# Optimization experiments

Hardware: AMD Instinct MI355X
Metric: run time of the kernel (lower is better)

The kernel has to match this reference:

```python
import jax, jax.numpy as jnp
import numpy as np

B, S, HID, QK, H = 2, 2048, 2048, 2048, 16
DK, DV = QK // H, HID // H
EPS = 1e-5


def setup_inputs() -> dict:
    key = jax.random.key(0)
    ks = jax.random.split(key, 8)
    sd = 1.0 / np.sqrt(HID)
    inp = {
        "x": jax.random.normal(ks[0], (B, S, HID), jnp.float32),
        "wq": jax.random.normal(ks[1], (HID, QK), jnp.float32) * sd,
        "bq": jnp.zeros((QK,), jnp.float32),
        "wk": jax.random.normal(ks[2], (HID, QK), jnp.float32) * sd,
        "bk": jnp.zeros((QK,), jnp.float32),
        "wv": jax.random.normal(ks[3], (HID, HID), jnp.float32) * sd,
        "bv": jnp.zeros((HID,), jnp.float32),
        "wg": jax.random.normal(ks[4], (HID, HID), jnp.float32) * sd,
        "bg": jnp.zeros((HID,), jnp.float32),
        "wo": jax.random.normal(ks[5], (HID, HID), jnp.float32) * sd,
        "bo": jnp.zeros((HID,), jnp.float32),
        "gn_w": jnp.ones((HID,), jnp.float32),
        "gn_b": jnp.zeros((HID,), jnp.float32),
        # RetNet default gammas: 1 - exp(linspace(log(1/32), log(1/512), H))
        "gamma": 1.0 - jnp.exp(jnp.linspace(-np.log(32.0), -np.log(512.0), H)).astype(jnp.float32),
    }
    return inp


def reference(x, wq, bq, wk, bk, wv, bv, wg, bg, wo, bo, gn_w, gn_b, gamma):
    b, s, hid = x.shape
    h = gamma.shape[0]
    dk = wq.shape[1] // h
    dv = hid // h
    # projections + head split -> (b, h, s, d)
    q = (x @ wq + bq).reshape(b, s, h, dk).transpose(0, 2, 1, 3)
    k = (x @ wk + bk).reshape(b, s, h, dk).transpose(0, 2, 1, 3)
    v = (x @ wv + bv).reshape(b, s, h, dv).transpose(0, 2, 1, 3)
    # causal decay mask: gamma^(n-m) for n >= m else 0  -> (h, s, s)
    idx = jnp.arange(s)
    diff = idx[:, None] - idx[None, :]
    expn = jnp.maximum(diff, 0).astype(x.dtype)
    dmask = jnp.where(diff >= 0, gamma[:, None, None] ** expn, 0.0)
    # parallel retention
    scores = jnp.einsum('bhnd,bhmd->bhnm', q, k) * dmask
    ret = jnp.einsum('bhnm,bhmv->bhnv', scores, v)  # (b, h, s, dv)
    # GroupNorm(num_groups=h) over (b, hid, s): stats per (b, head) over (s, dv)
    mean = ret.mean(axis=(2, 3), keepdims=True)
    var = ((ret - mean) ** 2).mean(axis=(2, 3), keepdims=True)
    norm = (ret - mean) * jax.lax.rsqrt(var + EPS)
    norm = norm * gn_w.reshape(h, dv)[None, :, None, :] + gn_b.reshape(h, dv)[None, :, None, :]
    ro = norm.transpose(0, 2, 1, 3).reshape(b, s, hid)  # (b, s, hid)
    gate = jax.nn.silu(x @ wg + bg)
    out = (gate * ro) @ wo + bo
    return out
```

## Files before the change

### kernel.cpp

```cpp
#include <hip/hip_runtime.h>
#include <cstdint>
#include <cstddef>

#define DEVI __device__ __forceinline__

typedef unsigned short u16;
typedef __bf16 bf16_t;
typedef bf16_t bf16x8 __attribute__((ext_vector_type(8)));
typedef float f32x4 __attribute__((ext_vector_type(4)));

constexpr int BB = 2, SS = 2048, HID = 2048, NH = 16, DK = 128, DV = 128;
constexpr int KD = HID;

DEVI u16 f2bf(float f) {
  union { float f; uint32_t u; } v; v.f = f;
  uint32_t u = v.u;
  uint32_t r = u + 0x7FFFu + ((u >> 16) & 1u);
  return (u16)(r >> 16);
}
DEVI float bf2f(u16 h) {
  union { uint32_t u; float f; } v; v.u = ((uint32_t)h) << 16;
  return v.f;
}
DEVI f32x4 mfma16(bf16x8 a, bf16x8 b, f32x4 c) {
  return __builtin_amdgcn_mfma_f32_16x16x32_bf16(a, b, c, 0, 0, 0);
}
DEVI void gload16(const u16* g, u16* l) {
  __builtin_amdgcn_global_load_lds(
      (const __attribute__((address_space(1))) uint32_t*)g,
      (__attribute__((address_space(3))) uint32_t*)l, 16, 0, 0);
}

__global__ __launch_bounds__(256) void castx_kernel(
    const float* __restrict__ x, u16* __restrict__ xb)
{
  size_t i = ((size_t)blockIdx.x * 256 + threadIdx.x) * 8;
  float4 a = *(const float4*)(x + i);
  float4 b = *(const float4*)(x + i + 4);
  ushort4 lo, hi;
  lo.x = f2bf(a.x); lo.y = f2bf(a.y); lo.z = f2bf(a.z); lo.w = f2bf(a.w);
  hi.x = f2bf(b.x); hi.y = f2bf(b.y); hi.z = f2bf(b.z); hi.w = f2bf(b.w);
  *(ushort4*)(xb + i) = lo;
  *(ushort4*)(xb + i + 4) = hi;
}

__global__ __launch_bounds__(256) void wtrans_kernel(
    const float* __restrict__ wq, const float* __restrict__ wk,
    const float* __restrict__ wv, const float* __restrict__ wg,
    const float* __restrict__ wo, u16* __restrict__ wt)
{
  __shared__ float t[32][33];
  const float* srcs[5] = {wq, wk, wv, wg, wo};
  const float* W = srcs[blockIdx.z];
  u16* dst = wt + (size_t)blockIdx.z * (size_t)KD * HID;
  int tx = threadIdx.x, ty = threadIdx.y;
  int c0 = blockIdx.x * 32, r0 = blockIdx.y * 32;
#pragma unroll
  for (int i = 0; i < 4; ++i)
    t[ty + i * 8][tx] = W[(size_t)(r0 + ty + i * 8) * HID + c0 + tx];
  __syncthreads();
#pragma unroll
  for (int i = 0; i < 4; ++i) {
    int n = c0 + ty + i * 8;
    int k = r0 + tx;
    dst[(size_t)n * KD + k] = f2bf(t[tx][ty + i * 8]);
  }
}

DEVI void stage256(const u16* __restrict__ A, const u16* __restrict__ Bt,
                   int m0, int n0, int kt, u16* sa, u16* sb, int tid)
{
#pragma unroll
  for (int i = 0; i < 4; ++i) {
    int c = i * 512 + tid;
    int row = c >> 3, scol = c & 7, dcol = scol ^ (row & 7);
    gload16(A + (size_t)(m0 + row) * KD + kt * 64 + dcol * 8, sa + c * 8);
  }
#pragma unroll
  for (int i = 0; i < 4; ++i) {
    int c = i * 512 + tid;
    int row = c >> 3, scol = c & 7, dcol = scol ^ (row & 7);
    gload16(Bt + (size_t)(n0 + row) * KD + kt * 64 + dcol * 8, sb + c * 8);
  }
}

DEVI void gemm256(const u16* __restrict__ A, const u16* __restrict__ Bt,
                  int m0, int n0, char* smem, f32x4 (&acc)[8][4])
{
  const int tid = threadIdx.x, lane = tid & 63, wave = tid >> 6;
  const int wr = wave >> 2, wc = wave & 3;
  const int lhi = lane >> 4, llo = lane & 15;

  stage256(A, Bt, m0, n0, 0, (u16*)smem, (u16*)(smem + 65536), tid);
  asm volatile("s_waitcnt vmcnt(0)" ::: "memory");
  __syncthreads();

  for (int kt = 0; kt < KD / 64; ++kt) {
    char* cA = smem + (kt & 1) * 32768;
    char* cB = smem + 65536 + (kt & 1) * 32768;
    if (kt + 1 < KD / 64) {
      u16* nA = (u16*)(smem + ((kt + 1) & 1) * 32768);
      u16* nB = (u16*)(smem + 65536 + ((kt + 1) & 1) * 32768);
      stage256(A, Bt, m0, n0, kt + 1, nA, nB, tid);
    }
    __builtin_amdgcn_s_setprio(1);
#pragma unroll
    for (int ks = 0; ks < 2; ++ks) {
      const int kb = ks * 64 + lhi * 16;
      bf16x8 bfr[4];
#pragma unroll
      for (int ni = 0; ni < 4; ++ni) {
        int row = wc * 64 + ni * 16 + llo;
        bfr[ni] = *(const bf16x8*)(cB + row * 128 + (kb ^ ((row & 7) << 4)));
      }
#pragma unroll
      for (int mi = 0; mi < 8; ++mi) {
        int row = wr * 128 + mi * 16 + llo;
        bf16x8 af = *(const bf16x8*)(cA + row * 128 + (kb ^ ((row & 7) << 4)));
#pragma unroll
        for (int ni = 0; ni < 4; ++ni)
          acc[mi][ni] = mfma16(af, bfr[ni], acc[mi][ni]);
      }
    }
    __builtin_amdgcn_s_setprio(0);
    asm volatile("s_waitcnt vmcnt(0)" ::: "memory");
    __syncthreads();
  }
}

__global__ __launch_bounds__(512, 2) void proj_kernel(
    const u16* __restrict__ xb, const u16* __restrict__ wtBase,
    const float* __restrict__ bq, const float* __restrict__ bk,
    const float* __restrict__ bv, const float* __restrict__ bg,
    u16* __restrict__ qb, u16* __restrict__ kb,
    u16* __restrict__ vtb, u16* __restrict__ gb)
{
  __shared__ __align__(16) char smem[131072];
  const int z = blockIdx.z;
  const u16* Bt = wtBase + (size_t)z * (size_t)KD * HID;
  f32x4 acc[8][4];
  const f32x4 zero = {0.f, 0.f, 0.f, 0.f};
#pragma unroll
  for (int mi = 0; mi < 8; ++mi)
#pragma unroll
    for (int ni = 0; ni < 4; ++ni) acc[mi][ni] = zero;

  const int m0 = blockIdx.x * 256, n0 = blockIdx.y * 256;
  gemm256(xb, Bt, m0, n0, smem, acc);

  const int tid = threadIdx.x, lane = tid & 63, wave = tid >> 6;
  const int wr = wave >> 2, wc = wave & 3;
  const int lhi = lane >> 4, llo = lane & 15;
  const float* bias = (z == 0) ? bq : (z == 1) ? bk : (z == 2) ? bv : bg;

  if (z == 2) {
#pragma unroll
    for (int mi = 0; mi < 8; ++mi) {
#pragma unroll
      for (int ni = 0; ni < 4; ++ni) {
        int row0 = m0 + wr * 128 + mi * 16 + lhi * 4;
        int n = n0 + wc * 64 + ni * 16 + llo;
        float bsn = bias[n];
        int b = row0 >> 11, s0 = row0 & (SS - 1);
        int h = n >> 7, j = n & 127;
        ushort4 hv;
        hv.x = f2bf(acc[mi][ni][0] + bsn);
        hv.y = f2bf(acc[mi][ni][1] + bsn);
        hv.z = f2bf(acc[mi][ni][2] + bsn);
        hv.w = f2bf(acc[mi][ni][3] + bsn);
        *(ushort4*)(vtb + ((size_t)((b * NH + h) * DV + j)) * SS + s0) = hv;
      }
    }
  } else {
    u16* Lb = (u16*)smem;
#pragma unroll
    for (int mi = 0; mi < 8; ++mi) {
#pragma unroll
      for (int ni = 0; ni < 4; ++ni) {
        int colL = wc * 64 + ni * 16 + llo;
        float bsn = bias[n0 + colL];
#pragma unroll
        for (int r = 0; r < 4; ++r) {
          int rowL = wr * 128 + mi * 16 + lhi * 4 + r;
          float c = acc[mi][ni][r] + bsn;
          if (z == 3) c = c / (1.0f + expf(-c));
          Lb[rowL * 256 + (colL ^ (((rowL >> 2) & 3) << 4))] = f2bf(c);
        }
      }
    }
    __syncthreads();
    int rr = tid & 255, chh = tid >> 8;
    int m = m0 + rr, b = m >> 11, s = m & (SS - 1);
    int swz = ((rr >> 2) & 3) << 4;
#pragma unroll
    for (int jj = 0; jj < 16; ++jj) {
      int c0 = chh * 128 + jj * 8;
      uint4 v = *(const uint4*)&Lb[rr * 256 + (c0 ^ swz)];
      int n = n0 + c0;
      if (z == 3) {
        *(uint4*)(gb + (size_t)m * HID + n) = v;
      } else {
        int h = n >> 7, j2 = n & 127;
        u16* dst = (z == 0) ? qb : kb;
        *(uint4*)(dst + ((size_t)((b * NH + h) * SS + s)) * DK + j2) = v;
      }
    }
  }
}

__global__ __launch_bounds__(256) void retention_kernel(
    const u16* __restrict__ qb, const u16* __restrict__ kb,
    const u16* __restrict__ vtb, const float* __restrict__ gamma,
    float* __restrict__ ret, float* __restrict__ stats)
{
  __shared__ __align__(16) char smemR[81920];
  __shared__ float red[8];

  const int bh = blockIdx.y;
  const int n0 = blockIdx.x * 128;
  const int h = bh & (NH - 1);
  const float lg2 = log2f(gamma[h]);

  const int tid = threadIdx.x, lane = tid & 63, wave = tid >> 6;
  const int lhi = lane >> 4, llo = lane & 15;
  const int qrow = n0 + wave * 32;

  const u16* qbase = qb + ((size_t)bh * SS + qrow) * DK;
  bf16x8 aq[2][4];
#pragma unroll
  for (int mi = 0; mi < 2; ++mi)
#pragma unroll
    for (int ks = 0; ks < 4; ++ks)
      aq[mi][ks] = *(const bf16x8*)(qbase + (size_t)(mi * 16 + llo) * DK + ks * 32 + lhi * 8);

  float rdec[2][4];
#pragma unroll
  for (int mi = 0; mi < 2; ++mi)
#pragma unroll
    for (int r = 0; r < 4; ++r)
      rdec[mi][r] = exp2f(lg2 * (float)(qrow + mi * 16 + lhi * 4 + r));

  const f32x4 zero = {0.f, 0.f, 0.f, 0.f};
  f32x4 oacc[2][8];
#pragma unroll
  for (int mi = 0; mi < 2; ++mi)
#pragma unroll
    for (int nj = 0; nj < 8; ++nj) oacc[mi][nj] = zero;

  const u16* kbase = kb + (size_t)bh * SS * DK;
  const u16* vbase = vtb + (size_t)bh * DV * SS;
  const int mtiles = n0 / 64 + 2;

  auto stageKV = [&](int mbase, u16* sk, u16* sv) {
#pragma unroll
    for (int i = 0; i < 4; ++i) {
      int c = i * 256 + tid;
      int row = c >> 4, scol = c & 15, dcol = scol ^ (row & 15);
      gload16(kbase + (size_t)(mbase + row) * DK + dcol * 8, sk + c * 8);
    }
#pragma unroll
    for (int i = 0; i < 4; ++i) {
      int c = i * 256 + tid;
      int row = c >> 3, scol = c & 7, dcol = scol ^ (row & 7);
      gload16(vbase + (size_t)row * SS + mbase + dcol * 8, sv + c * 8);
    }
  };

  stageKV(0, (u16*)smemR, (u16*)(smemR + 32768));
  asm volatile("s_waitcnt vmcnt(0)" ::: "memory");
  __syncthreads();

  for (int mt = 0; mt < mtiles; ++mt) {
    const int m0 = mt * 64;
    char* cK = smemR + (mt & 1) * 16384;
    char* cV = smemR + 32768 + (mt & 1) * 16384;
    if (mt + 1 < mtiles)
      stageKV(m0 + 64, (u16*)(smemR + ((mt + 1) & 1) * 16384),
              (u16*)(smemR + 32768 + ((mt + 1) & 1) * 16384));

    f32x4 sacc[2][4];
#pragma unroll
    for (int mi = 0; mi < 2; ++mi)
#pragma unroll
      for (int ni = 0; ni < 4; ++ni) sacc[mi][ni] = zero;
    __builtin_amdgcn_s_setprio(1);
#pragma unroll
    for (int ks = 0; ks < 4; ++ks) {
      const int kbyte = ks * 64 + lhi * 16;
      bf16x8 bk_[4];
#pragma unroll
      for (int ni = 0; ni < 4; ++ni) {
        int row = ni * 16 + llo;
        bk_[ni] = *(const bf16x8*)(cK + row * 256 + (kbyte ^ ((row & 15) << 4)));
      }
#pragma unroll
      for (int mi = 0; mi < 2; ++mi)
#pragma unroll
        for (int ni = 0; ni < 4; ++ni)
          sacc[mi][ni] = mfma16(aq[mi][ks], bk_[ni], sacc[mi][ni]);
    }
    __builtin_amdgcn_s_setprio(0);

    float cfac[4];
#pragma unroll
    for (int ni = 0; ni < 4; ++ni)
      cfac[ni] = exp2f(-lg2 * (float)(m0 + ni * 16 + llo));
    const bool masked = (m0 + 63 > qrow);
    char* myP = smemR + 65536 + wave * 4096;
#pragma unroll
    for (int mi = 0; mi < 2; ++mi) {
#pragma unroll
      for (int ni = 0; ni < 4; ++ni) {
#pragma unroll
        for (int r = 0; r < 4; ++r) {
          int prow = mi * 16 + lhi * 4 + r;
          int pcol = ni * 16 + llo;
          float w = rdec[mi][r] * cfac[ni];
          if (masked && (qrow + prow < m0 + pcol)) w = 0.0f;
          float p = sacc[mi][ni][r] * w;
          *(u16*)(myP + prow * 128 + ((pcol * 2) ^ ((prow & 7) << 4))) = f2bf(p);
        }
      }
    }

    __builtin_amdgcn_s_setprio(1);
#pragma unroll
    for (int ks2 = 0; ks2 < 2; ++ks2) {
      const int kbyte = ks2 * 64 + lhi * 16;
      bf16x8 pa[2];
#pragma unroll
      for (int mi = 0; mi < 2; ++mi) {
        int row = mi * 16 + llo;
        pa[mi] = *(const bf16x8*)(myP + row * 128 + (kbyte ^ ((row & 7) << 4)));
      }
#pragma unroll
      for (int nj = 0; nj < 8; ++nj) {
        int row = nj * 16 + llo;
        bf16x8 vb = *(const bf16x8*)(cV + row * 128 + (kbyte ^ ((row & 7) << 4)));
#pragma unroll
        for (int mi = 0; mi < 2; ++mi)
          oacc[mi][nj] = mfma16(pa[mi], vb, oacc[mi][nj]);
      }
    }
    __builtin_amdgcn_s_setprio(0);
    asm volatile("s_waitcnt vmcnt(0)" ::: "memory");
    __syncthreads();
  }

  float lsum = 0.f, lsq = 0.f;
  float* rbase = ret + ((size_t)bh * SS + qrow) * DV;
#pragma unroll
  for (int mi = 0; mi < 2; ++mi) {
#pragma unroll
    for (int nj = 0; nj < 8; ++nj) {
      int prow0 = mi * 16 + lhi * 4;
      int j = nj * 16 + llo;
#pragma unroll
      for (int r = 0; r < 4; ++r) {
        float v = oacc[mi][nj][r];
        rbase[(size_t)(prow0 + r) * DV + j] = v;
        lsum += v; lsq += v * v;
      }
    }
  }
#pragma unroll
  for (int off = 32; off > 0; off >>= 1) {
    lsum += __shfl_down(lsum, off, 64);
    lsq  += __shfl_down(lsq,  off, 64);
  }
  if (lane == 0) { red[wave * 2] = lsum; red[wave * 2 + 1] = lsq; }
  __syncthreads();
  if (tid == 0) {
    float s = red[0] + red[2] + red[4] + red[6];
    float q = red[1] + red[3] + red[5] + red[7];
    atomicAdd(&stats[bh * 2], s);
    atomicAdd(&stats[bh * 2 + 1], q);
  }
}

__global__ __launch_bounds__(256) void normgate_kernel(
    const float* __restrict__ ret, const u16* __restrict__ gb,
    const float* __restrict__ stats, const float* __restrict__ gn_w,
    const float* __restrict__ gn_b, u16* __restrict__ a2)
{
  const int idx4 = (blockIdx.x * 256 + threadIdx.x) * 4;
  const int bh = idx4 >> 18;
  const int rem = idx4 & (SS * DV - 1);
  const int s = rem >> 7;
  const int dv = rem & (DV - 1);
  const float inv = 1.0f / (float)(SS * DV);
  float mean = stats[bh * 2] * inv;
  float var = stats[bh * 2 + 1] * inv - mean * mean;
  float rstd = rsqrtf(var + 1e-5f);
  const int b = bh >> 4, h = bh & (NH - 1);
  const int hd = h * DV + dv;
  float4 rv = *(const float4*)(ret + idx4);
  float4 w4 = *(const float4*)(gn_w + hd);
  float4 b4 = *(const float4*)(gn_b + hd);
  size_t gidx = ((size_t)(b * SS + s)) * HID + hd;
  ushort4 g4 = *(const ushort4*)(gb + gidx);
  ushort4 o;
  o.x = f2bf(bf2f(g4.x) * ((rv.x - mean) * rstd * w4.x + b4.x));
  o.y = f2bf(bf2f(g4.y) * ((rv.y - mean) * rstd * w4.y + b4.y));
  o.z = f2bf(bf2f(g4.z) * ((rv.z - mean) * rstd * w4.z + b4.z));
  o.w = f2bf(bf2f(g4.w) * ((rv.w - mean) * rstd * w4.w + b4.w));
  *(ushort4*)(a2 + gidx) = o;
}

__global__ __launch_bounds__(512, 2) void final_kernel(
    const u16* __restrict__ a2, const u16* __restrict__ woT,
    const float* __restrict__ bo, float* __restrict__ out)
{
  __shared__ __align__(16) char smem[131072];
  f32x4 acc[8][4];
  const f32x4 zero = {0.f, 0.f, 0.f, 0.f};
#pragma unroll
  for (int mi = 0; mi < 8; ++mi)
#pragma unroll
    for (int ni = 0; ni < 4; ++ni) acc[mi][ni] = zero;

  const int m0 = blockIdx.x * 256, n0 = blockIdx.y * 256;
  gemm256(a2, woT, m0, n0, smem, acc);

  const int tid = threadIdx.x, lane = tid & 63, wave = tid >> 6;
  const int wr = wave >> 2, wc = wave & 3;
  const int lhi = lane >> 4, llo = lane & 15;
  float* Lf = (float*)smem;

#pragma unroll
  for (int pass = 0; pass < 2; ++pass) {
    if ((wc >> 1) == pass) {
#pragma unroll
      for (int mi = 0; mi < 8; ++mi) {
#pragma unroll
        for (int ni = 0; ni < 4; ++ni) {
          int colL = (wc & 1) * 64 + ni * 16 + llo;
          float bn = bo[n0 + pass * 128 + colL];
#pragma unroll
          for (int r = 0; r < 4; ++r) {
            int rowL = wr * 128 + mi * 16 + lhi * 4 + r;
            Lf[rowL * 128 + (colL ^ (((rowL >> 2) & 1) << 4))] =
                acc[mi][ni][r] + bn;
          }
        }
      }
    }
    __syncthreads();
    int rr = tid & 255, chh = tid >> 8;
    int m = m0 + rr;
    int swz = ((rr >> 2) & 1) << 4;
#pragma unroll
    for (int jj = 0; jj < 16; ++jj) {
      int c0 = chh * 64 + jj * 4;
      float4 v = *(const float4*)&Lf[rr * 128 + (c0 ^ swz)];
      *(float4*)(out + (size_t)m * HID + n0 + pass * 128 + c0) = v;
    }
    __syncthreads();
  }
}

extern "C" void kernel_launch(void* const* d_in, const int* in_sizes, int n_in,
                              void* d_out, int out_size, void* d_ws, size_t ws_size,
                              hipStream_t stream) {
  const float* x    = (const float*)d_in[0];
  const float* wq   = (const float*)d_in[1];
  const float* bq   = (const float*)d_in[2];
  const float* wk   = (const float*)d_in[3];
  const float* bk   = (const float*)d_in[4];
  const float* wv   = (const float*)d_in[5];
  const float* bv   = (const float*)d_in[6];
  const float* wg   = (const float*)d_in[7];
  const float* bg   = (const float*)d_in[8];
  const float* wo   = (const float*)d_in[9];
  const float* bo   = (const float*)d_in[10];
  const float* gn_w = (const float*)d_in[11];
  const float* gn_b = (const float*)d_in[12];
  const float* gam  = (const float*)d_in[13];

  char* ws = (char*)d_ws;
  u16* wT    = (u16*)(ws);
  u16* qb    = (u16*)(ws + 41943040);
  u16* kbuf  = (u16*)(ws + 58720256);
  u16* vtb   = (u16*)(ws + 75497472);
  u16* gb    = (u16*)(ws + 92274688);
  float* ret = (float*)(ws + 109051904);
  float* st  = (float*)(ws + 142606336);
  u16* a2    = qb;
  u16* xb    = (u16*)ret;

  hipMemsetAsync(st, 0, 256, stream);
  castx_kernel<<<4096, 256, 0, stream>>>(x, xb);
  wtrans_kernel<<<dim3(64, 64, 5), dim3(32, 8), 0, stream>>>(wq, wk, wv, wg, wo, wT);
  proj_kernel<<<dim3(16, 8, 4), 512, 0, stream>>>(xb, wT, bq, bk, bv, bg, qb, kbuf, vtb, gb);
  retention_kernel<<<dim3(16, 32), 256, 0, stream>>>(qb, kbuf, vtb, gam, ret, st);
  normgate_kernel<<<16384, 256, 0, stream>>>(ret, gb, st, gn_w, gn_b, a2);
  final_kernel<<<dim3(16, 8), 512, 0, stream>>>(a2, wT + (size_t)4 * KD * HID, bo, (float*)d_out);
}
```

Before: 552.9 us.

## Replace double-buffered GEMM with 4-stage K=32 ring and retile output GEMM

```diff
diff --git a/kernel.cpp b/kernel.cpp
--- a/kernel.cpp
+++ b/kernel.cpp
@@ -30,6 +30,8 @@
       (const __attribute__((address_space(1))) uint32_t*)g,
       (__attribute__((address_space(3))) uint32_t*)l, 16, 0, 0);
 }
+
+#define WAITVM(N) asm volatile("s_waitcnt vmcnt(" #N ")" ::: "memory")
 
 __global__ __launch_bounds__(256) void castx_kernel(
     const float* __restrict__ x, u16* __restrict__ xb)
@@ -67,64 +69,74 @@
   }
 }
 
-DEVI void stage256(const u16* __restrict__ A, const u16* __restrict__ Bt,
-                   int m0, int n0, int kt, u16* sa, u16* sb, int tid)
-{
-#pragma unroll
-  for (int i = 0; i < 4; ++i) {
-    int c = i * 512 + tid;
-    int row = c >> 3, scol = c & 7, dcol = scol ^ (row & 7);
-    gload16(A + (size_t)(m0 + row) * KD + kt * 64 + dcol * 8, sa + c * 8);
-  }
-#pragma unroll
-  for (int i = 0; i < 4; ++i) {
-    int c = i * 512 + tid;
-    int row = c >> 3, scol = c & 7, dcol = scol ^ (row & 7);
-    gload16(Bt + (size_t)(n0 + row) * KD + kt * 64 + dcol * 8, sb + c * 8);
-  }
-}
-
-DEVI void gemm256(const u16* __restrict__ A, const u16* __restrict__ Bt,
-                  int m0, int n0, char* smem, f32x4 (&acc)[8][4])
-{
+template<int BM, int BN>
+DEVI void stage32(const u16* __restrict__ A, const u16* __restrict__ Bt,
+                  int m0, int n0, int kt, char* lds, int tid)
+{
+  char* sA = lds + (kt & 3) * (BM * 64);
+  char* sB = lds + 4 * BM * 64 + (kt & 3) * (BN * 64);
+  const u16* srcA = A + (size_t)m0 * KD + kt * 32;
+#pragma unroll
+  for (int i = 0; i < BM / 128; ++i) {
+    int ch = i * 512 + tid;
+    int r2 = ch >> 3, sub = (ch >> 2) & 1, cp = ch & 3;
+    int c = cp ^ (r2 & 3), r = r2 * 2 + sub;
+    gload16(srcA + (size_t)r * KD + c * 8, (u16*)(sA + ch * 16));
+  }
+  const u16* srcB = Bt + (size_t)n0 * KD + kt * 32;
+#pragma unroll
+  for (int i = 0; i < BN / 128; ++i) {
+    int ch = i * 512 + tid;
+    int r2 = ch >> 3, sub = (ch >> 2) & 1, cp = ch & 3;
+    int c = cp ^ (r2 & 3), r = r2 * 2 + sub;
+    gload16(srcB + (size_t)r * KD + c * 8, (u16*)(sB + ch * 16));
+  }
+}
+
+DEVI int swz_addr(int r, int lhi) {
+  return (r >> 1) * 128 + (r & 1) * 64 + ((lhi ^ ((r >> 1) & 3)) << 4);
+}
+
+template<int BM, int BN, int WRN, int WCN, int MF, int NF>
+DEVI void gemm_ring(const u16* __restrict__ A, const u16* __restrict__ Bt,
+                    int m0, int n0, char* lds, f32x4 (&acc)[MF][NF])
+{
+  constexpr int NTk = KD / 32;
+  constexpr int LPB = (BM + BN) / 128;
   const int tid = threadIdx.x, lane = tid & 63, wave = tid >> 6;
-  const int wr = wave >> 2, wc = wave & 3;
+  const int wrb = (wave / WCN) * (BM / WRN);
+  const int wcb = (wave % WCN) * 64;
   const int lhi = lane >> 4, llo = lane & 15;
 
-  stage256(A, Bt, m0, n0, 0, (u16*)smem, (u16*)(smem + 65536), tid);
-  asm volatile("s_waitcnt vmcnt(0)" ::: "memory");
-  __syncthreads();
-
-  for (int kt = 0; kt < KD / 64; ++kt) {
-    char* cA = smem + (kt & 1) * 32768;
-    char* cB = smem + 65536 + (kt & 1) * 32768;
-    if (kt + 1 < KD / 64) {
-      u16* nA = (u16*)(smem + ((kt + 1) & 1) * 32768);
-      u16* nB = (u16*)(smem + 65536 + ((kt + 1) & 1) * 32768);
-      stage256(A, Bt, m0, n0, kt + 1, nA, nB, tid);
-    }
+  stage32<BM, BN>(A, Bt, m0, n0, 0, lds, tid);
+  stage32<BM, BN>(A, Bt, m0, n0, 1, lds, tid);
+  stage32<BM, BN>(A, Bt, m0, n0, 2, lds, tid);
+  if constexpr (LPB == 4) WAITVM(8); else WAITVM(6);
+  __builtin_amdgcn_s_barrier();
+  __builtin_amdgcn_sched_barrier(0);
+
+  for (int kt = 0; kt < NTk; ++kt) {
+    if (kt + 3 < NTk) stage32<BM, BN>(A, Bt, m0, n0, kt + 3, lds, tid);
+    char* sA = lds + (kt & 3) * (BM * 64);
+    char* sB = lds + 4 * BM * 64 + (kt & 3) * (BN * 64);
     __builtin_amdgcn_s_setprio(1);
-#pragma unroll
-    for (int ks = 0; ks < 2; ++ks) {
-      const int kb = ks * 64 + lhi * 16;
-      bf16x8 bfr[4];
-#pragma unroll
-      for (int ni = 0; ni < 4; ++ni) {
-        int row = wc * 64 + ni * 16 + llo;
-        bfr[ni] = *(const bf16x8*)(cB + row * 128 + (kb ^ ((row & 7) << 4)));
-      }
-#pragma unroll
-      for (int mi = 0; mi < 8; ++mi) {
-        int row = wr * 128 + mi * 16 + llo;
-        bf16x8 af = *(const bf16x8*)(cA + row * 128 + (kb ^ ((row & 7) << 4)));
-#pragma unroll
-        for (int ni = 0; ni < 4; ++ni)
-          acc[mi][ni] = mfma16(af, bfr[ni], acc[mi][ni]);
-      }
+    bf16x8 bfr[NF];
+#pragma unroll
+    for (int ni = 0; ni < NF; ++ni)
+      bfr[ni] = *(const bf16x8*)(sB + swz_addr(wcb + ni * 16 + llo, lhi));
+#pragma unroll
+    for (int mi = 0; mi < MF; ++mi) {
+      bf16x8 af = *(const bf16x8*)(sA + swz_addr(wrb + mi * 16 + llo, lhi));
+#pragma unroll
+      for (int ni = 0; ni < NF; ++ni)
+        acc[mi][ni] = mfma16(af, bfr[ni], acc[mi][ni]);
     }
     __builtin_amdgcn_s_setprio(0);
-    asm volatile("s_waitcnt vmcnt(0)" ::: "memory");
-    __syncthreads();
+    if (kt < NTk - 3)       { if constexpr (LPB == 4) WAITVM(8); else WAITVM(6); }
+    else if (kt == NTk - 3) { if constexpr (LPB == 4) WAITVM(4); else WAITVM(3); }
+    else                    WAITVM(0);
+    __builtin_amdgcn_s_barrier();
+    __builtin_amdgcn_sched_barrier(0);
   }
 }
 
@@ -146,33 +158,39 @@
     for (int ni = 0; ni < 4; ++ni) acc[mi][ni] = zero;
 
   const int m0 = blockIdx.x * 256, n0 = blockIdx.y * 256;
-  gemm256(xb, Bt, m0, n0, smem, acc);
+  gemm_ring<256, 256, 2, 4, 8, 4>(xb, Bt, m0, n0, smem, acc);
 
   const int tid = threadIdx.x, lane = tid & 63, wave = tid >> 6;
   const int wr = wave >> 2, wc = wave & 3;
   const int lhi = lane >> 4, llo = lane & 15;
   const float* bias = (z == 0) ? bq : (z == 1) ? bk : (z == 2) ? bv : bg;
+  u16* Lb = (u16*)smem;
 
   if (z == 2) {
 #pragma unroll
     for (int mi = 0; mi < 8; ++mi) {
 #pragma unroll
       for (int ni = 0; ni < 4; ++ni) {
-        int row0 = m0 + wr * 128 + mi * 16 + lhi * 4;
-        int n = n0 + wc * 64 + ni * 16 + llo;
-        float bsn = bias[n];
-        int b = row0 >> 11, s0 = row0 & (SS - 1);
-        int h = n >> 7, j = n & 127;
-        ushort4 hv;
-        hv.x = f2bf(acc[mi][ni][0] + bsn);
-        hv.y = f2bf(acc[mi][ni][1] + bsn);
-        hv.z = f2bf(acc[mi][ni][2] + bsn);
-        hv.w = f2bf(acc[mi][ni][3] + bsn);
-        *(ushort4*)(vtb + ((size_t)((b * NH + h) * DV + j)) * SS + s0) = hv;
-      }
+        int nl = wc * 64 + ni * 16 + llo;
+        float bsn = bias[n0 + nl];
+#pragma unroll
+        for (int r = 0; r < 4; ++r) {
+          int sl = wr * 128 + mi * 16 + lhi * 4 + r;
+          Lb[nl * 256 + (sl ^ ((nl & 7) << 3))] = f2bf(acc[mi][ni][r] + bsn);
+        }
+      }
+    }
+    __syncthreads();
+    const int b = m0 >> 11, sbase = m0 & (SS - 1), h0 = n0 >> 7;
+#pragma unroll
+    for (int jj = 0; jj < 16; ++jj) {
+      int id = jj * 512 + tid;
+      int nl = id >> 5, c8 = id & 31;
+      uint4 v = *(const uint4*)&Lb[nl * 256 + ((c8 * 8) ^ ((nl & 7) << 3))];
+      int h = h0 + (nl >> 7), j = nl & 127;
+      *(uint4*)(vtb + ((size_t)((b * NH + h) * DV + j)) * SS + sbase + c8 * 8) = v;
     }
   } else {
-    u16* Lb = (u16*)smem;
 #pragma unroll
     for (int mi = 0; mi < 8; ++mi) {
 #pragma unroll
@@ -184,19 +202,18 @@
           int rowL = wr * 128 + mi * 16 + lhi * 4 + r;
           float c = acc[mi][ni][r] + bsn;
           if (z == 3) c = c / (1.0f + expf(-c));
-          Lb[rowL * 256 + (colL ^ (((rowL >> 2) & 3) << 4))] = f2bf(c);
+          Lb[rowL * 256 + (colL ^ ((rowL & 7) << 3))] = f2bf(c);
         }
       }
     }
     __syncthreads();
-    int rr = tid & 255, chh = tid >> 8;
-    int m = m0 + rr, b = m >> 11, s = m & (SS - 1);
-    int swz = ((rr >> 2) & 3) << 4;
 #pragma unroll
     for (int jj = 0; jj < 16; ++jj) {
-      int c0 = chh * 128 + jj * 8;
-      uint4 v = *(const uint4*)&Lb[rr * 256 + (c0 ^ swz)];
-      int n = n0 + c0;
+      int id = jj * 512 + tid;
+      int rr = id >> 5, c8 = id & 31;
+      uint4 v = *(const uint4*)&Lb[rr * 256 + ((c8 * 8) ^ ((rr & 7) << 3))];
+      int m = m0 + rr, b = m >> 11, s = m & (SS - 1);
+      int n = n0 + c8 * 8;
       if (z == 3) {
         *(uint4*)(gb + (size_t)m * HID + n) = v;
       } else {
@@ -412,50 +429,42 @@
     const float* __restrict__ bo, float* __restrict__ out)
 {
   __shared__ __align__(16) char smem[131072];
-  f32x4 acc[8][4];
+  f32x4 acc[4][4];
   const f32x4 zero = {0.f, 0.f, 0.f, 0.f};
 #pragma unroll
-  for (int mi = 0; mi < 8; ++mi)
+  for (int mi = 0; mi < 4; ++mi)
 #pragma unroll
     for (int ni = 0; ni < 4; ++ni) acc[mi][ni] = zero;
 
-  const int m0 = blockIdx.x * 256, n0 = blockIdx.y * 256;
-  gemm256(a2, woT, m0, n0, smem, acc);
+  const int m0 = blockIdx.x * 256, n0 = blockIdx.y * 128;
+  gemm_ring<256, 128, 4, 2, 4, 4>(a2, woT, m0, n0, smem, acc);
 
   const int tid = threadIdx.x, lane = tid & 63, wave = tid >> 6;
-  const int wr = wave >> 2, wc = wave & 3;
+  const int wr = wave >> 1, wc = wave & 1;
   const int lhi = lane >> 4, llo = lane & 15;
   float* Lf = (float*)smem;
 
 #pragma unroll
-  for (int pass = 0; pass < 2; ++pass) {
-    if ((wc >> 1) == pass) {
-#pragma unroll
-      for (int mi = 0; mi < 8; ++mi) {
-#pragma unroll
-        for (int ni = 0; ni < 4; ++ni) {
-          int colL = (wc & 1) * 64 + ni * 16 + llo;
-          float bn = bo[n0 + pass * 128 + colL];
-#pragma unroll
-          for (int r = 0; r < 4; ++r) {
-            int rowL = wr * 128 + mi * 16 + lhi * 4 + r;
-            Lf[rowL * 128 + (colL ^ (((rowL >> 2) & 1) << 4))] =
-                acc[mi][ni][r] + bn;
-          }
-        }
-      }
-    }
-    __syncthreads();
-    int rr = tid & 255, chh = tid >> 8;
-    int m = m0 + rr;
-    int swz = ((rr >> 2) & 1) << 4;
-#pragma unroll
-    for (int jj = 0; jj < 16; ++jj) {
-      int c0 = chh * 64 + jj * 4;
-      float4 v = *(const float4*)&Lf[rr * 128 + (c0 ^ swz)];
-      *(float4*)(out + (size_t)m * HID + n0 + pass * 128 + c0) = v;
-    }
-    __syncthreads();
+  for (int mi = 0; mi < 4; ++mi) {
+#pragma unroll
+    for (int ni = 0; ni < 4; ++ni) {
+      int colL = wc * 64 + ni * 16 + llo;
+      float bn = bo[n0 + colL];
+#pragma unroll
+      for (int r = 0; r < 4; ++r) {
+        int rowL = wr * 64 + mi * 16 + lhi * 4 + r;
+        Lf[rowL * 128 + (colL ^ ((rowL & 7) << 2))] = acc[mi][ni][r] + bn;
+      }
+    }
+  }
+  __syncthreads();
+#pragma unroll
+  for (int jj = 0; jj < 16; ++jj) {
+    int id = jj * 512 + tid;
+    int row = id >> 5, c4 = id & 31;
+    int col = c4 * 4;
+    float4 v = *(const float4*)&Lf[row * 128 + (col ^ ((row & 7) << 2))];
+    *(float4*)(out + (size_t)(m0 + row) * HID + n0 + col) = v;
   }
 }
 
@@ -494,5 +503,5 @@
   proj_kernel<<<dim3(16, 8, 4), 512, 0, stream>>>(xb, wT, bq, bk, bv, bg, qb, kbuf, vtb, gb);
   retention_kernel<<<dim3(16, 32), 256, 0, stream>>>(qb, kbuf, vtb, gam, ret, st);
   normgate_kernel<<<16384, 256, 0, stream>>>(ret, gb, st, gn_w, gn_b, a2);
-  final_kernel<<<dim3(16, 8), 512, 0, stream>>>(a2, wT + (size_t)4 * KD * HID, bo, (float*)d_out);
-}
+  final_kernel<<<dim3(16, 16), 512, 0, stream>>>(a2, wT + (size_t)4 * KD * HID, bo, (float*)d_out);
+}
```

Measured after the change: 521.3 us. 5.7% less time.
